# Performance work log

Measured on AMD Instinct MI355X. Metric: run time of the kernel, lower is better.

## Reference

```python
import jax, jax.numpy as jnp
import numpy as np

T, D_IN, D_OUT, E = 8192, 1024, 1024, 8
LN_EPS = 1e-5


def setup_inputs() -> dict:
    key = jax.random.key(0)
    k1, k2, k3 = jax.random.split(key, 3)
    x = jax.random.normal(k1, (T, D_IN), dtype=jnp.float32)
    # tokens are pre-sorted by expert; equal load => capacity = T // E per expert
    expert_frequency = jnp.full((E,), T // E, dtype=jnp.int64)
    # per-expert Linear(input_dim, output_dim) params
    W = jax.random.normal(k2, (E, D_IN, D_OUT), dtype=jnp.float32) / np.sqrt(D_IN)
    b = jax.random.normal(k3, (E, D_OUT), dtype=jnp.float32) * 0.02
    # per-expert LayerNorm(output_dim) affine params
    ln_gamma = jnp.ones((E, D_OUT), dtype=jnp.float32)
    ln_beta = jnp.zeros((E, D_OUT), dtype=jnp.float32)
    return {
        "expert_ordered_input": x,
        "expert_frequency": expert_frequency,
        "W": W,
        "b": b,
        "ln_gamma": ln_gamma,
        "ln_beta": ln_beta,
    }


def reference(expert_ordered_input, expert_frequency, W, b, ln_gamma, ln_beta):
    # Grouped-GEMM form of: split tokens by expert_frequency, apply per-expert
    # LayerBlock (Linear -> relu -> LayerNorm), then concat along token dim.
    # Frequencies are equal (capacity = T // E), so the ragged split is a reshape.
    x = expert_ordered_input
    n_tok, d_in = x.shape
    n_exp = W.shape[0]
    cap = n_tok // n_exp  # static capacity per expert
    xe = x.reshape(n_exp, cap, d_in)                       # [E, cap, d_in]
    h = jnp.einsum("ecd,edf->ecf", xe, W) + b[:, None, :]  # [E, cap, d_out]
    h = jax.nn.relu(h)
    mu = jnp.mean(h, axis=-1, keepdims=True)
    var = jnp.var(h, axis=-1, keepdims=True)
    hn = (h - mu) * jax.lax.rsqrt(var + LN_EPS)
    out = hn * ln_gamma[:, None, :] + ln_beta[:, None, :]
    return out.reshape(n_tok, -1)                          # concat over experts
```

## Files before the change

### kernel.cpp

```cpp
#include <hip/hip_runtime.h>
#include <hip/hip_bf16.h>
#include <stdint.h>

#define T_TOK 8192
#define DIN   1024
#define DOUT  1024
#define NEXP  8
#define CAP   1024
#define LN_EPS 1e-5f

#define BM 128
#define BN 128
#define BK 32

typedef __attribute__((ext_vector_type(8))) short short8;
typedef __attribute__((ext_vector_type(4))) float f32x4;

__device__ __forceinline__ unsigned short f2bf(float f) {
    union { float f; unsigned int u; } v; v.f = f;
    unsigned int u = v.u;
    unsigned int r = u + 0x7FFFu + ((u >> 16) & 1u);
    return (unsigned short)(r >> 16);
}
__device__ __forceinline__ float bf2f(unsigned short h) {
    union { unsigned int u; float f; } v; v.u = ((unsigned int)h) << 16;
    return v.f;
}

__device__ __forceinline__ void gld16(void* l, const void* g) {
    __builtin_amdgcn_global_load_lds(
        (const __attribute__((address_space(1))) unsigned int*)(uintptr_t)g,
        (__attribute__((address_space(3))) unsigned int*)(uintptr_t)l,
        16, 0, 0);
}

__global__ __launch_bounds__(256) void prep_kernel(
    const float* __restrict__ X, const float* __restrict__ W,
    unsigned short* __restrict__ Xb, unsigned short* __restrict__ Wt) {
    __shared__ float tile[64][65];
    int blk = blockIdx.x;
    int tid = threadIdx.x;
    if (blk < 2048) {
        int e  = blk & 7;
        int r0 = (blk >> 3) * 4;
        size_t base = ((size_t)(e * CAP + r0)) * 256 + tid;
#pragma unroll
        for (int q = 0; q < 4; q++) {
            size_t i = base + (size_t)q * 256;
            float4 v = ((const float4*)X)[i];
            ushort4 o;
            o.x = f2bf(v.x); o.y = f2bf(v.y); o.z = f2bf(v.z); o.w = f2bf(v.w);
            ((ushort4*)Xb)[i] = o;
        }
    } else {
        int t  = blk - 2048;
        int e  = t & 7;
        int tl = t >> 3;
        int k0 = (tl >> 4) * 64;
        int n0 = (tl & 15) * 64;
        const float* Wp = W + (size_t)e * DIN * DOUT;
        unsigned short* Wtp = Wt + (size_t)e * DIN * DOUT;
        int rr = tid >> 4;
        int cc = tid & 15;
#pragma unroll
        for (int q = 0; q < 4; q++) {
            int k = rr + q * 16;
            float4 v = *(const float4*)(Wp + (size_t)(k0 + k) * DOUT + n0 + cc * 4);
            tile[k][cc * 4 + 0] = v.x;
            tile[k][cc * 4 + 1] = v.y;
            tile[k][cc * 4 + 2] = v.z;
            tile[k][cc * 4 + 3] = v.w;
        }
        __syncthreads();
#pragma unroll
        for (int q = 0; q < 4; q++) {
            int n = rr + q * 16;
            ushort4 o;
            o.x = f2bf(tile[cc * 4 + 0][n]);
            o.y = f2bf(tile[cc * 4 + 1][n]);
            o.z = f2bf(tile[cc * 4 + 2][n]);
            o.w = f2bf(tile[cc * 4 + 3][n]);
            *(ushort4*)(Wtp + (size_t)(n0 + n) * DIN + k0 + cc * 4) = o;
        }
    }
}

__global__ __launch_bounds__(256, 2) void gemm6_kernel(
    const unsigned short* __restrict__ Xb,
    const unsigned short* __restrict__ Wt,
    const float* __restrict__ Bias,
    unsigned short* __restrict__ Hb,
    float2* __restrict__ P)
{
    __shared__ unsigned short As[2][2][BM * BK];
    __shared__ unsigned short Bs[2][2][BN * BK];

    int blk = blockIdx.x;
    int e   = blk & 7;
    int mi  = blk >> 6;
    int m0  = mi * BM;
    int ni  = (blk >> 3) & 7;
    int n0  = ni * BN;

    int tid  = threadIdx.x;
    int wave = tid >> 6;
    int lane = tid & 63;
    int wm   = (wave >> 1) * 64;
    int wn   = (wave & 1) * 64;
    int lrow = lane & 15;
    int quad = lane >> 4;

    const unsigned short* Ag = Xb + (size_t)(e * CAP + m0) * DIN;
    const unsigned short* Bg = Wt + (size_t)e * DOUT * DIN + (size_t)n0 * DIN;

    int l0 = tid;
    int l1 = tid + 256;
    int ar0 = l0 >> 2, ac0 = (l0 & 3) * 8;
    int ar1 = l1 >> 2, ac1 = (l1 & 3) * 8;

    f32x4 acc[4][4];
#pragma unroll
    for (int i = 0; i < 4; i++)
#pragma unroll
        for (int j = 0; j < 4; j++)
            acc[i][j] = (f32x4)(0.0f);

#define STAGE(buf, kb)                                                        \
    {                                                                         \
        _Pragma("unroll")                                                     \
        for (int s = 0; s < 2; s++) {                                         \
            int k0 = (kb) + s * BK;                                           \
            gld16(&As[buf][s][l0 * 8], Ag + (size_t)ar0 * DIN + k0 + ac0);    \
            gld16(&As[buf][s][l1 * 8], Ag + (size_t)ar1 * DIN + k0 + ac1);    \
            gld16(&Bs[buf][s][l0 * 8], Bg + (size_t)ar0 * DIN + k0 + ac0);    \
            gld16(&Bs[buf][s][l1 * 8], Bg + (size_t)ar1 * DIN + k0 + ac1);    \
        }                                                                     \
    }

#define COMPUTE(buf)                                                          \
    {                                                                         \
        _Pragma("unroll")                                                     \
        for (int s = 0; s < 2; s++) {                                         \
            short8 af[4], bfr[4];                                             \
            _Pragma("unroll")                                                 \
            for (int i = 0; i < 4; i++)                                       \
                af[i] = *(const short8*)&As[buf][s][(wm + i * 16 + lrow) * BK + quad * 8]; \
            _Pragma("unroll")                                                 \
            for (int j = 0; j < 4; j++)                                       \
                bfr[j] = *(const short8*)&Bs[buf][s][(wn + j * 16 + lrow) * BK + quad * 8]; \
            _Pragma("unroll")                                                 \
            for (int i = 0; i < 4; i++)                                       \
                _Pragma("unroll")                                             \
                for (int j = 0; j < 4; j++)                                   \
                    acc[i][j] = __builtin_amdgcn_mfma_f32_16x16x32_bf16(af[i], bfr[j], acc[i][j], 0, 0, 0); \
        }                                                                     \
    }

    STAGE(0, 0);
    __syncthreads();
    for (int kb = 64; kb < 960; kb += 128) {
        STAGE(1, kb);
        COMPUTE(0);
        __syncthreads();
        STAGE(0, kb + 64);
        COMPUTE(1);
        __syncthreads();
    }
    STAGE(1, 960);
    COMPUTE(0);
    __syncthreads();
    COMPUTE(1);

#undef STAGE
#undef COMPUTE

    float bias[4];
#pragma unroll
    for (int j = 0; j < 4; j++)
        bias[j] = Bias[e * DOUT + n0 + wn + j * 16 + lrow];

    int tok0  = e * CAP + m0 + wm;
    int chunk = ni * 2 + (wave & 1);

#pragma unroll
    for (int i = 0; i < 4; i++) {
#pragma unroll
        for (int r = 0; r < 4; r++) {
            float s = 0.f, ss = 0.f;
#pragma unroll
            for (int j = 0; j < 4; j++) {
                float v = fmaxf(acc[i][j][r] + bias[j], 0.f);
                acc[i][j][r] = v;
                s += v;
                ss = fmaf(v, v, ss);
            }
#pragma unroll
            for (int m = 1; m <= 8; m <<= 1) {
                s  += __shfl_xor(s, m);
                ss += __shfl_xor(ss, m);
            }
            int grow = tok0 + i * 16 + quad * 4 + r;
            if (lrow == 0)
                P[(size_t)grow * 16 + chunk] = make_float2(s, ss);
#pragma unroll
            for (int j = 0; j < 4; j++) {
                int gcol = n0 + wn + j * 16 + lrow;
                Hb[(size_t)grow * DOUT + gcol] = f2bf(acc[i][j][r]);
            }
        }
    }
}

__global__ __launch_bounds__(256) void ln2_kernel(
    const unsigned short* __restrict__ Hb,
    const float2* __restrict__ P,
    const float* __restrict__ G,
    const float* __restrict__ Bt,
    float* __restrict__ Out)
{
    int blk = blockIdx.x;
    int e   = blk & 7;
    int r2  = (blk >> 3) * 2;
    int row0 = e * CAP + r2;
    int tid = threadIdx.x;
    __shared__ float sh[2][2];

    if (tid < 32) {
        int r = tid >> 4;
        float2 p = P[(size_t)(row0 + r) * 16 + (tid & 15)];
        float s = p.x, ss = p.y;
#pragma unroll
        for (int m = 1; m <= 8; m <<= 1) {
            s  += __shfl_xor(s, m);
            ss += __shfl_xor(ss, m);
        }
        if ((tid & 15) == 0) {
            float mu  = s * (1.0f / DOUT);
            float var = fmaxf(ss * (1.0f / DOUT) - mu * mu, 0.f);
            sh[r][0] = mu;
            sh[r][1] = rsqrtf(var + LN_EPS);
        }
    }
    __syncthreads();

    float4 g = ((const float4*)G)[e * 256 + tid];
    float4 b = ((const float4*)Bt)[e * 256 + tid];
#pragma unroll
    for (int r = 0; r < 2; r++) {
        float mu = sh[r][0], rs = sh[r][1];
        ushort4 hb = ((const ushort4*)Hb)[(size_t)(row0 + r) * 256 + tid];
        float4 y;
        y.x = (bf2f(hb.x) - mu) * rs * g.x + b.x;
        y.y = (bf2f(hb.y) - mu) * rs * g.y + b.y;
        y.z = (bf2f(hb.z) - mu) * rs * g.z + b.z;
        y.w = (bf2f(hb.w) - mu) * rs * g.w + b.w;
        ((float4*)Out)[(size_t)(row0 + r) * 256 + tid] = y;
    }
}

extern "C" void kernel_launch(void* const* d_in, const int* in_sizes, int n_in,
                              void* d_out, int out_size, void* d_ws, size_t ws_size,
                              hipStream_t stream) {
    const float* x  = (const float*)d_in[0];
    const float* W  = (const float*)d_in[2];
    const float* b  = (const float*)d_in[3];
    const float* g  = (const float*)d_in[4];
    const float* be = (const float*)d_in[5];
    float* out = (float*)d_out;

    const size_t WT_BYTES = (size_t)NEXP * DIN * DOUT * 2;
    const size_t XB_BYTES = (size_t)T_TOK * DIN * 2;
    const size_t P_BYTES  = (size_t)T_TOK * 16 * 8;
    const size_t HB_BYTES = (size_t)T_TOK * DOUT * 2;
    if (ws_size < WT_BYTES + XB_BYTES + P_BYTES + HB_BYTES) return;

    unsigned short* Wt = (unsigned short*)d_ws;
    unsigned short* Xb = (unsigned short*)((char*)d_ws + WT_BYTES);
    float2* P = (float2*)((char*)d_ws + WT_BYTES + XB_BYTES);
    unsigned short* Hb = (unsigned short*)((char*)d_ws + WT_BYTES + XB_BYTES + P_BYTES);

    dim3 tb(256);
    prep_kernel<<<dim3(4096), tb, 0, stream>>>(x, W, Xb, Wt);
    gemm6_kernel<<<dim3(512), tb, 0, stream>>>(Xb, Wt, b, Hb, P);
    ln2_kernel<<<dim3(4096), tb, 0, stream>>>(Hb, P, g, be, out);
}
```

Before: 147.3 us.

## Restructure grouped GEMM into 256x128 tiles with triple-buffered swizzled LDS pipeline

The GEMM now uses 512-thread blocks covering 256x128 output tiles with BK=64, so the grid drops to 256 blocks. Shared memory becomes a three-stage ring buffer filled by direct global-to-LDS loads, using an XOR swizzle on the k-group to avoid bank conflicts. The loop waits on explicit vmcnt counts with raw s_barrier and raises wave priority around the MFMA bursts. The goal is to hide load latency and reuse each B tile across more rows. The costs are more LDS per block (about 144KB), which may allow only one block per CU, and a tail of 256 blocks on a 256-CU part.

```diff
diff --git a/kernel.cpp b/kernel.cpp
--- a/kernel.cpp
+++ b/kernel.cpp
@@ -9,9 +9,12 @@
 #define CAP   1024
 #define LN_EPS 1e-5f
 
-#define BM 128
+#define BM 256
 #define BN 128
-#define BK 32
+#define BKT 64
+#define ABUF (BM * BKT)
+#define BBUF (BN * BKT)
+#define BUFSZ (ABUF + BBUF)
 
 typedef __attribute__((ext_vector_type(8))) short short8;
 typedef __attribute__((ext_vector_type(4))) float f32x4;
@@ -85,38 +88,41 @@
     }
 }
 
-__global__ __launch_bounds__(256, 2) void gemm6_kernel(
+__global__ __launch_bounds__(512, 2) void gemm7_kernel(
     const unsigned short* __restrict__ Xb,
     const unsigned short* __restrict__ Wt,
     const float* __restrict__ Bias,
     unsigned short* __restrict__ Hb,
     float2* __restrict__ P)
 {
-    __shared__ unsigned short As[2][2][BM * BK];
-    __shared__ unsigned short Bs[2][2][BN * BK];
+    __shared__ unsigned short lds[3 * BUFSZ];
 
     int blk = blockIdx.x;
     int e   = blk & 7;
+    int ni  = (blk >> 3) & 7;
     int mi  = blk >> 6;
     int m0  = mi * BM;
-    int ni  = (blk >> 3) & 7;
     int n0  = ni * BN;
 
-    int tid  = threadIdx.x;
-    int wave = tid >> 6;
-    int lane = tid & 63;
+    int t    = threadIdx.x;
+    int wave = t >> 6;
+    int lane = t & 63;
     int wm   = (wave >> 1) * 64;
     int wn   = (wave & 1) * 64;
     int lrow = lane & 15;
     int quad = lane >> 4;
+    int l7   = lrow & 7;
 
     const unsigned short* Ag = Xb + (size_t)(e * CAP + m0) * DIN;
     const unsigned short* Bg = Wt + (size_t)e * DOUT * DIN + (size_t)n0 * DIN;
 
-    int l0 = tid;
-    int l1 = tid + 256;
-    int ar0 = l0 >> 2, ac0 = (l0 & 3) * 8;
-    int ar1 = l1 >> 2, ac1 = (l1 & 3) * 8;
+    int trow   = t >> 3;
+    int kg_src = (t & 7) ^ (trow & 7);
+
+    int aoff0 = (wm + lrow) * BKT + ((quad) ^ l7) * 8;
+    int aoff1 = (wm + lrow) * BKT + ((4 + quad) ^ l7) * 8;
+    int boff0 = (wn + lrow) * BKT + ((quad) ^ l7) * 8;
+    int boff1 = (wn + lrow) * BKT + ((4 + quad) ^ l7) * 8;
 
     f32x4 acc[4][4];
 #pragma unroll
@@ -125,54 +131,104 @@
         for (int j = 0; j < 4; j++)
             acc[i][j] = (f32x4)(0.0f);
 
-#define STAGE(buf, kb)                                                        \
-    {                                                                         \
-        _Pragma("unroll")                                                     \
-        for (int s = 0; s < 2; s++) {                                         \
-            int k0 = (kb) + s * BK;                                           \
-            gld16(&As[buf][s][l0 * 8], Ag + (size_t)ar0 * DIN + k0 + ac0);    \
-            gld16(&As[buf][s][l1 * 8], Ag + (size_t)ar1 * DIN + k0 + ac1);    \
-            gld16(&Bs[buf][s][l0 * 8], Bg + (size_t)ar0 * DIN + k0 + ac0);    \
-            gld16(&Bs[buf][s][l1 * 8], Bg + (size_t)ar1 * DIN + k0 + ac1);    \
-        }                                                                     \
-    }
-
-#define COMPUTE(buf)                                                          \
-    {                                                                         \
-        _Pragma("unroll")                                                     \
-        for (int s = 0; s < 2; s++) {                                         \
-            short8 af[4], bfr[4];                                             \
-            _Pragma("unroll")                                                 \
-            for (int i = 0; i < 4; i++)                                       \
-                af[i] = *(const short8*)&As[buf][s][(wm + i * 16 + lrow) * BK + quad * 8]; \
-            _Pragma("unroll")                                                 \
-            for (int j = 0; j < 4; j++)                                       \
-                bfr[j] = *(const short8*)&Bs[buf][s][(wn + j * 16 + lrow) * BK + quad * 8]; \
-            _Pragma("unroll")                                                 \
-            for (int i = 0; i < 4; i++)                                       \
-                _Pragma("unroll")                                             \
-                for (int j = 0; j < 4; j++)                                   \
-                    acc[i][j] = __builtin_amdgcn_mfma_f32_16x16x32_bf16(af[i], bfr[j], acc[i][j], 0, 0, 0); \
-        }                                                                     \
-    }
-
-    STAGE(0, 0);
-    __syncthreads();
-    for (int kb = 64; kb < 960; kb += 128) {
-        STAGE(1, kb);
-        COMPUTE(0);
-        __syncthreads();
-        STAGE(0, kb + 64);
-        COMPUTE(1);
-        __syncthreads();
-    }
-    STAGE(1, 960);
-    COMPUTE(0);
-    __syncthreads();
-    COMPUTE(1);
-
-#undef STAGE
-#undef COMPUTE
+#define STAGE_H(bb, k0, h)                                                     \
+    {                                                                          \
+        unsigned short* Ab_ = &lds[(bb) * BUFSZ];                              \
+        unsigned short* Bb_ = &lds[(bb) * BUFSZ + ABUF];                       \
+        gld16(Ab_ + (((h) * 2 + 0) * 512 + t) * 8,                             \
+              Ag + (size_t)(((h) * 2 + 0) * 64 + trow) * DIN + (k0) + kg_src * 8); \
+        gld16(Ab_ + (((h) * 2 + 1) * 512 + t) * 8,                             \
+              Ag + (size_t)(((h) * 2 + 1) * 64 + trow) * DIN + (k0) + kg_src * 8); \
+        gld16(Bb_ + ((h) * 512 + t) * 8,                                       \
+              Bg + (size_t)((h) * 64 + trow) * DIN + (k0) + kg_src * 8);       \
+    }
+
+#define LOADFRAGS(bb, ao, bo)                                                  \
+    {                                                                          \
+        const unsigned short* Ab_ = &lds[(bb) * BUFSZ];                        \
+        const unsigned short* Bb_ = &lds[(bb) * BUFSZ + ABUF];                 \
+        _Pragma("unroll")                                                      \
+        for (int i = 0; i < 4; i++)                                            \
+            af[i] = *(const short8*)&Ab_[(ao) + i * 16 * BKT];                 \
+        _Pragma("unroll")                                                      \
+        for (int j = 0; j < 4; j++)                                            \
+            bf[j] = *(const short8*)&Bb_[(bo) + j * 16 * BKT];                 \
+    }
+
+#define MFMA16()                                                               \
+    {                                                                          \
+        __builtin_amdgcn_s_setprio(1);                                         \
+        _Pragma("unroll")                                                      \
+        for (int i = 0; i < 4; i++)                                            \
+            _Pragma("unroll")                                                  \
+            for (int j = 0; j < 4; j++)                                        \
+                acc[i][j] = __builtin_amdgcn_mfma_f32_16x16x32_bf16(           \
+                    af[i], bf[j], acc[i][j], 0, 0, 0);                         \
+        __builtin_amdgcn_s_setprio(0);                                         \
+    }
+
+#define BAR() __builtin_amdgcn_s_barrier()
+#define VMW(n) asm volatile("s_waitcnt vmcnt(" #n ")" ::: "memory")
+
+    STAGE_H(0, 0, 0);
+    STAGE_H(0, 0, 1);
+    STAGE_H(1, BKT, 0);
+    STAGE_H(1, BKT, 1);
+    VMW(6);
+    BAR();
+
+    int cur = 0, nxt = 1, fut = 2;
+    for (int p = 0; p < 14; ++p) {
+        int k2 = (p + 2) * BKT;
+        {
+            short8 af[4], bf[4];
+            LOADFRAGS(cur, aoff0, boff0);
+            STAGE_H(fut, k2, 0);
+            BAR();
+            MFMA16();
+            BAR();
+        }
+        {
+            short8 af[4], bf[4];
+            LOADFRAGS(cur, aoff1, boff1);
+            STAGE_H(fut, k2, 1);
+            BAR();
+            MFMA16();
+            VMW(6);
+            BAR();
+        }
+        int tmp = cur; cur = nxt; nxt = fut; fut = tmp;
+    }
+    {
+        short8 af[4], bf[4];
+        LOADFRAGS(cur, aoff0, boff0);
+        BAR(); MFMA16(); BAR();
+    }
+    {
+        short8 af[4], bf[4];
+        LOADFRAGS(cur, aoff1, boff1);
+        BAR(); MFMA16();
+        VMW(0);
+        BAR();
+    }
+    {
+        short8 af[4], bf[4];
+        LOADFRAGS(nxt, aoff0, boff0);
+        BAR(); MFMA16(); BAR();
+    }
+    {
+        short8 af[4], bf[4];
+        LOADFRAGS(nxt, aoff1, boff1);
+        BAR(); MFMA16();
+    }
+
+#undef STAGE_H
+#undef LOADFRAGS
+#undef MFMA16
+#undef BAR
+#undef VMW
+
+    asm volatile("" ::: "memory");
 
     float bias[4];
 #pragma unroll
@@ -279,8 +335,7 @@
     float2* P = (float2*)((char*)d_ws + WT_BYTES + XB_BYTES);
     unsigned short* Hb = (unsigned short*)((char*)d_ws + WT_BYTES + XB_BYTES + P_BYTES);
 
-    dim3 tb(256);
-    prep_kernel<<<dim3(4096), tb, 0, stream>>>(x, W, Xb, Wt);
-    gemm6_kernel<<<dim3(512), tb, 0, stream>>>(Xb, Wt, b, Hb, P);
-    ln2_kernel<<<dim3(4096), tb, 0, stream>>>(Hb, P, g, be, out);
-}
+    prep_kernel<<<dim3(4096), dim3(256), 0, stream>>>(x, W, Xb, Wt);
+    gemm7_kernel<<<dim3(256), dim3(512), 0, stream>>>(Xb, Wt, b, Hb, P);
+    ln2_kernel<<<dim3(4096), dim3(256), 0, stream>>>(Hb, P, g, be, out);
+}
```

Result: no change. 146.5 us (-0.5%).
